# Optimization experiments

Hardware: AMD Instinct MI355X
Metric: run time of the kernel (lower is better)

The kernel has to match this reference:

```python
import jax, jax.numpy as jnp
import numpy as np

N_WIRES = 8
DIM = 2 ** N_WIRES  # 256
NUM_HEADS = 4

def _cnot_ring_perm():
    # Compose CNOT(w, w+1) for w=0..6 then CNOT(7, 0) into one basis permutation.
    # Wire 0 is the most-significant bit of the basis index.
    perm = np.arange(DIM)
    pairs = [(w, w + 1) for w in range(N_WIRES - 1)] + [(N_WIRES - 1, 0)]
    j = np.arange(DIM)
    for c, t in pairs:
        ctrl = (j >> (N_WIRES - 1 - c)) & 1
        M = j ^ (ctrl << (N_WIRES - 1 - t))  # flip target bit where control=1 (involution)
        perm = perm[M]
    return perm

PERM = _cnot_ring_perm()
# SIGNS[i, w] = <i|Z_w|i> = 1 - 2*bit_w(i)
SIGNS = np.array([[1.0 - 2.0 * ((i >> (N_WIRES - 1 - w)) & 1) for w in range(N_WIRES)]
                  for i in range(DIM)], dtype=np.float32)

def setup_inputs() -> dict:
    key = jax.random.key(0)
    k1, k2, k3 = jax.random.split(key, 3)
    x = jax.random.normal(k1, (16, 4096, N_WIRES), jnp.float32)  # rotation angles per token
    theta = jax.random.normal(k2, (N_WIRES,), jnp.float32)       # trainable RX params
    w_combine = jax.random.normal(k3, (N_WIRES, N_WIRES), jnp.float32) / np.float32(np.sqrt(N_WIRES))
    b_combine = jnp.zeros((N_WIRES,), jnp.float32)
    return {"x": x, "theta": theta, "w_combine": w_combine, "b_combine": b_combine}

def _quantum_features(x, theta):
    # RX(x_i) then RX(theta_i) on wire i compose to RX(x_i + theta_i) acting on |0>.
    B, S, E = x.shape
    N = B * S
    phi = (x + theta).reshape(N, E)
    c = jnp.cos(0.5 * phi).astype(jnp.complex64)
    s = (-1j) * jnp.sin(0.5 * phi)          # RX|0> = cos(phi/2)|0> - i sin(phi/2)|1>
    wv = jnp.stack([c, s.astype(jnp.complex64)], axis=-1)  # (N, 8, 2)
    # Build product state via successive Kronecker products (wire 0 = MSB).
    state = jnp.ones((N, 1), jnp.complex64)
    for w in range(E):
        state = (state[:, :, None] * wv[:, w, None, :]).reshape(N, -1)  # (N, 2^(w+1))
    state = state[:, jnp.asarray(PERM)]      # apply the CNOT ring as one permutation
    probs = state.real ** 2 + state.imag ** 2  # (N, 256)
    return (probs @ jnp.asarray(SIGNS)).reshape(B, S, E)  # <Z_w> per token

def reference(x, theta, w_combine, b_combine):
    B, S, E = x.shape
    d_k = E // NUM_HEADS
    q = _quantum_features(x, theta)           # (B, S, 8); k = v = q in the source
    scores = jnp.einsum('bse,bte->bst', q, q) / np.float32(np.sqrt(d_k))
    attn = jax.nn.softmax(scores, axis=-1)    # dropout is identity in eval mode
    out = jnp.einsum('bst,bte->bse', attn, q)
    # Faithful to source: transpose(1,2).contiguous().view(B, S, E)
    out = jnp.swapaxes(out, 1, 2).reshape(B, S, E)
    return out @ w_combine.T + b_combine
```

## Files before the change

### kernel.cpp

```cpp
#include <hip/hip_runtime.h>
#include <math.h>


#define SEQ   4096
#define NB    16
#define SROWS 128
#define TPB   1024
#define NTG   4
#define TC    1024
#define NCH   (SEQ / TC)
#define TILES_PER_TG 8
#define KSTR  12
#define VSTR  1032

typedef _Float16 f16x4  __attribute__((ext_vector_type(4)));
typedef _Float16 f16x8  __attribute__((ext_vector_type(8)));
typedef float    f32x16 __attribute__((ext_vector_type(16)));
typedef __fp16   hf2    __attribute__((ext_vector_type(2)));

#if __has_builtin(__builtin_amdgcn_exp2f)
#define EXP2F(x) __builtin_amdgcn_exp2f(x)
#else
#define EXP2F(x) exp2f(x)
#endif

__global__ __launch_bounds__(TPB, 8)
void qattn_kernel(const float* __restrict__ x, const float* __restrict__ theta,
                  const float* __restrict__ wc, const float* __restrict__ bc,
                  float* __restrict__ out)
{
    __shared__ __align__(16) _Float16 kf[TC * KSTR];
    __shared__ __align__(16) _Float16 vt[9 * VSTR];
    float* part = (float*)kf;
    float* attn = (float*)vt;

    const int tid  = threadIdx.x;
    const int lane = tid & 63;
    const int wv   = tid >> 6;
    const int sub  = wv & 3;
    const int tg   = wv >> 2;
    const int l31  = lane & 31;
    const int hp   = lane >> 5;

    const int b  = blockIdx.x >> 5;
    const int S0 = (blockIdx.x & 31) * SROWS;
    const float* xb = x + (size_t)b * SEQ * 8;

    const int pos = (tid & ~12) | ((tid & 4) << 1) | ((tid & 8) >> 1);

    float th[8];
#pragma unroll
    for (int w = 0; w < 8; ++w) th[w] = theta[w];

    vt[8 * VSTR + tid] = (_Float16)1.0f;

    f16x4 qfrag;
    {
        const int s = S0 + sub * 32 + l31;
        const float4 xa  = *(const float4*)(xb + s * 8);
        const float4 xb4 = *(const float4*)(xb + s * 8 + 4);
        float c0 = __cosf(xa.x  + th[0]);
        float c1 = __cosf(xa.y  + th[1]);
        float c2 = __cosf(xa.z  + th[2]);
        float c3 = __cosf(xa.w  + th[3]);
        float c4 = __cosf(xb4.x + th[4]);
        float c5 = __cosf(xb4.y + th[5]);
        float c6 = __cosf(xb4.z + th[6]);
        float c7 = __cosf(xb4.w + th[7]);
        float p1 = c0 * c1, p2 = p1 * c2, p3 = p2 * c3, p4 = p3 * c4;
        float p5 = p4 * c5, p6 = p5 * c6, p7 = p6 * c7;
        float p0 = c1 * c2 * c3 * c4 * c5 * c6 * c7;
        const float sc = 0.70710678118654752f * 1.44269504088896341f;
        if (hp == 0)
            qfrag = (f16x4){(_Float16)(p0*sc), (_Float16)(p1*sc),
                            (_Float16)(p2*sc), (_Float16)(p3*sc)};
        else
            qfrag = (f16x4){(_Float16)(p4*sc), (_Float16)(p5*sc),
                            (_Float16)(p6*sc), (_Float16)(p7*sc)};
    }

    f32x16 o = {0.f,0.f,0.f,0.f,0.f,0.f,0.f,0.f,0.f,0.f,0.f,0.f,0.f,0.f,0.f,0.f};

    const int wr = (l31 < 8) ? l31 : 8;
    const _Float16* kfb = kf + l31 * KSTR + 4 * hp + (tg * TILES_PER_TG) * 32 * KSTR;
    const _Float16* vbb = vt + wr * VSTR + 8 * hp + tg * (TILES_PER_TG * 32);

    float4 pxa = *(const float4*)(xb + tid * 8);
    float4 pxb = *(const float4*)(xb + tid * 8 + 4);

    for (int ch = 0; ch < NCH; ++ch) {
        float c0 = __cosf(pxa.x + th[0]);
        float c1 = __cosf(pxa.y + th[1]);
        float c2 = __cosf(pxa.z + th[2]);
        float c3 = __cosf(pxa.w + th[3]);
        float c4 = __cosf(pxb.x + th[4]);
        float c5 = __cosf(pxb.y + th[5]);
        float c6 = __cosf(pxb.z + th[6]);
        float c7 = __cosf(pxb.w + th[7]);
        float p1 = c0 * c1, p2 = p1 * c2, p3 = p2 * c3, p4 = p3 * c4;
        float p5 = p4 * c5, p6 = p5 * c6, p7 = p6 * c7;
        float p0 = c1 * c2 * c3 * c4 * c5 * c6 * c7;
        _Float16 h0 = (_Float16)p0, h1 = (_Float16)p1, h2 = (_Float16)p2,
                 h3 = (_Float16)p3, h4 = (_Float16)p4, h5 = (_Float16)p5,
                 h6 = (_Float16)p6, h7 = (_Float16)p7;
        __syncthreads();
        {
            _Float16* krow = kf + tid * KSTR;
            *(f16x4*)(krow)     = (f16x4){h0, h1, h2, h3};
            *(f16x4*)(krow + 4) = (f16x4){h4, h5, h6, h7};
            vt[0 * VSTR + pos] = h0;
            vt[1 * VSTR + pos] = h1;
            vt[2 * VSTR + pos] = h2;
            vt[3 * VSTR + pos] = h3;
            vt[4 * VSTR + pos] = h4;
            vt[5 * VSTR + pos] = h5;
            vt[6 * VSTR + pos] = h6;
            vt[7 * VSTR + pos] = h7;
        }
        __syncthreads();
        {
            const int nt = ((ch + 1 < NCH) ? (ch + 1) * TC : ch * TC) + tid;
            pxa = *(const float4*)(xb + nt * 8);
            pxb = *(const float4*)(xb + nt * 8 + 4);
        }
#pragma unroll 4
        for (int i = 0; i < TILES_PER_TG; ++i) {
            f16x4 kfrag = *(const f16x4*)(kfb + i * 32 * KSTR);
            f32x16 cc = __builtin_amdgcn_mfma_f32_32x32x8f16(
                kfrag, qfrag, (f32x16){0.f,0.f,0.f,0.f,0.f,0.f,0.f,0.f,
                                       0.f,0.f,0.f,0.f,0.f,0.f,0.f,0.f}, 0, 0, 0);
#pragma unroll
            for (int h = 0; h < 2; ++h) {
                union { hf2 q[4]; f16x8 v; } pa;
                pa.q[0] = __builtin_amdgcn_cvt_pkrtz(EXP2F(cc[8*h+0]), EXP2F(cc[8*h+1]));
                pa.q[1] = __builtin_amdgcn_cvt_pkrtz(EXP2F(cc[8*h+2]), EXP2F(cc[8*h+3]));
                pa.q[2] = __builtin_amdgcn_cvt_pkrtz(EXP2F(cc[8*h+4]), EXP2F(cc[8*h+5]));
                pa.q[3] = __builtin_amdgcn_cvt_pkrtz(EXP2F(cc[8*h+6]), EXP2F(cc[8*h+7]));
                f16x8 vfrag = *(const f16x8*)(vbb + i * 32 + h * 16);
                o = __builtin_amdgcn_mfma_f32_32x32x16_f16(pa.v, vfrag, o, 0, 0, 0);
            }
        }
    }

    __syncthreads();
    if (l31 < 9) {
#pragma unroll
        for (int r = 0; r < 16; ++r) {
            const int sloc = sub * 32 + (r & 3) + 8 * (r >> 2) + 4 * hp;
            part[((tg * SROWS) + sloc) * 9 + l31] = o[r];
        }
    }
    __syncthreads();
    for (int idx = tid; idx < SROWS * 9; idx += TPB) {
        const int rr = idx / 9;
        const int w  = idx - rr * 9;
        float sm = 0.f;
#pragma unroll
        for (int g = 0; g < NTG; ++g) sm += part[((g * SROWS) + rr) * 9 + w];
        attn[rr * 9 + w] = sm;
    }
    __syncthreads();
    if (tid < SROWS * 8) {
        const int rr = tid >> 3;
        const int w  = tid & 7;
        attn[rr * 9 + w] = attn[rr * 9 + w] / attn[rr * 9 + 8];
    }
    __syncthreads();

    if (tid < SROWS) {
        const int e    = tid >> 4;
        const int nloc = tid & 15;
        const int r    = e * 512 + (S0 >> 3) + nloc;
        float y[8];
#pragma unroll
        for (int c = 0; c < 8; ++c) y[c] = attn[(nloc * 8 + c) * 9 + e];
        float oo[8];
#pragma unroll
        for (int k = 0; k < 8; ++k) {
            float a = bc[k];
#pragma unroll
            for (int c = 0; c < 8; ++c) a += y[c] * wc[k * 8 + c];
            oo[k] = a;
        }
        float4* op = (float4*)(out + ((size_t)b * SEQ + r) * 8);
        op[0] = make_float4(oo[0], oo[1], oo[2], oo[3]);
        op[1] = make_float4(oo[4], oo[5], oo[6], oo[7]);
    }
}

extern "C" void kernel_launch(void* const* d_in, const int* in_sizes, int n_in,
                              void* d_out, int out_size, void* d_ws, size_t ws_size,
                              hipStream_t stream)
{
    const float* x  = (const float*)d_in[0];
    const float* th = (const float*)d_in[1];
    const float* wc = (const float*)d_in[2];
    const float* bc = (const float*)d_in[3];
    float* out = (float*)d_out;

    qattn_kernel<<<dim3(NB * (SEQ / SROWS)), dim3(TPB), 0, stream>>>(x, th, wc, bc, out);
}
```

Before: 92.37 us.

## Double-buffer K/V tiles in shared memory with halved chunk size

Splits the key/value chunk from 1024 to 512 tokens and double-buffers the shared-memory K and V tiles. Each iteration stages the next chunk while computing MFMAs on the current one, leaving one barrier per chunk instead of two. Only half the threads do the staging, and the loop runs twice as many chunks. Shared-memory footprint stays about the same, so occupancy should be unchanged.

After: 88.19 us. -4.5%, faster.

```diff
diff --git a/kernel.cpp b/kernel.cpp
--- a/kernel.cpp
+++ b/kernel.cpp
@@ -7,11 +7,13 @@
 #define SROWS 128
 #define TPB   1024
 #define NTG   4
-#define TC    1024
+#define TC    512
 #define NCH   (SEQ / TC)
-#define TILES_PER_TG 8
+#define TPT   4
 #define KSTR  12
-#define VSTR  1032
+#define VSTR  520
+#define KFSZ  (TC * KSTR)
+#define VTSZ  (9 * VSTR)
 
 typedef _Float16 f16x4  __attribute__((ext_vector_type(4)));
 typedef _Float16 f16x8  __attribute__((ext_vector_type(8)));
@@ -29,8 +31,8 @@
                   const float* __restrict__ wc, const float* __restrict__ bc,
                   float* __restrict__ out)
 {
-    __shared__ __align__(16) _Float16 kf[TC * KSTR];
-    __shared__ __align__(16) _Float16 vt[9 * VSTR];
+    __shared__ __align__(16) _Float16 kf[2 * KFSZ];
+    __shared__ __align__(16) _Float16 vt[2 * VTSZ];
     float* part = (float*)kf;
     float* attn = (float*)vt;
 
@@ -51,8 +53,6 @@
     float th[8];
 #pragma unroll
     for (int w = 0; w < 8; ++w) th[w] = theta[w];
-
-    vt[8 * VSTR + tid] = (_Float16)1.0f;
 
     f16x4 qfrag;
     {
@@ -79,52 +79,64 @@
                             (_Float16)(p6*sc), (_Float16)(p7*sc)};
     }
 
-    f32x16 o = {0.f,0.f,0.f,0.f,0.f,0.f,0.f,0.f,0.f,0.f,0.f,0.f,0.f,0.f,0.f,0.f};
-
-    const int wr = (l31 < 8) ? l31 : 8;
-    const _Float16* kfb = kf + l31 * KSTR + 4 * hp + (tg * TILES_PER_TG) * 32 * KSTR;
-    const _Float16* vbb = vt + wr * VSTR + 8 * hp + tg * (TILES_PER_TG * 32);
-
-    float4 pxa = *(const float4*)(xb + tid * 8);
-    float4 pxb = *(const float4*)(xb + tid * 8 + 4);
-
-    for (int ch = 0; ch < NCH; ++ch) {
-        float c0 = __cosf(pxa.x + th[0]);
-        float c1 = __cosf(pxa.y + th[1]);
-        float c2 = __cosf(pxa.z + th[2]);
-        float c3 = __cosf(pxa.w + th[3]);
-        float c4 = __cosf(pxb.x + th[4]);
-        float c5 = __cosf(pxb.y + th[5]);
-        float c6 = __cosf(pxb.z + th[6]);
-        float c7 = __cosf(pxb.w + th[7]);
+    auto stage = [&](int buf, float4 xa, float4 xb4) {
+        float c0 = __cosf(xa.x  + th[0]);
+        float c1 = __cosf(xa.y  + th[1]);
+        float c2 = __cosf(xa.z  + th[2]);
+        float c3 = __cosf(xa.w  + th[3]);
+        float c4 = __cosf(xb4.x + th[4]);
+        float c5 = __cosf(xb4.y + th[5]);
+        float c6 = __cosf(xb4.z + th[6]);
+        float c7 = __cosf(xb4.w + th[7]);
         float p1 = c0 * c1, p2 = p1 * c2, p3 = p2 * c3, p4 = p3 * c4;
         float p5 = p4 * c5, p6 = p5 * c6, p7 = p6 * c7;
         float p0 = c1 * c2 * c3 * c4 * c5 * c6 * c7;
         _Float16 h0 = (_Float16)p0, h1 = (_Float16)p1, h2 = (_Float16)p2,
                  h3 = (_Float16)p3, h4 = (_Float16)p4, h5 = (_Float16)p5,
                  h6 = (_Float16)p6, h7 = (_Float16)p7;
-        __syncthreads();
-        {
-            _Float16* krow = kf + tid * KSTR;
-            *(f16x4*)(krow)     = (f16x4){h0, h1, h2, h3};
-            *(f16x4*)(krow + 4) = (f16x4){h4, h5, h6, h7};
-            vt[0 * VSTR + pos] = h0;
-            vt[1 * VSTR + pos] = h1;
-            vt[2 * VSTR + pos] = h2;
-            vt[3 * VSTR + pos] = h3;
-            vt[4 * VSTR + pos] = h4;
-            vt[5 * VSTR + pos] = h5;
-            vt[6 * VSTR + pos] = h6;
-            vt[7 * VSTR + pos] = h7;
-        }
-        __syncthreads();
-        {
-            const int nt = ((ch + 1 < NCH) ? (ch + 1) * TC : ch * TC) + tid;
-            pxa = *(const float4*)(xb + nt * 8);
-            pxb = *(const float4*)(xb + nt * 8 + 4);
-        }
-#pragma unroll 4
-        for (int i = 0; i < TILES_PER_TG; ++i) {
+        _Float16* krow = kf + buf * KFSZ + tid * KSTR;
+        *(f16x4*)(krow)     = (f16x4){h0, h1, h2, h3};
+        *(f16x4*)(krow + 4) = (f16x4){h4, h5, h6, h7};
+        _Float16* vb = vt + buf * VTSZ + pos;
+        vb[0 * VSTR] = h0;
+        vb[1 * VSTR] = h1;
+        vb[2 * VSTR] = h2;
+        vb[3 * VSTR] = h3;
+        vb[4 * VSTR] = h4;
+        vb[5 * VSTR] = h5;
+        vb[6 * VSTR] = h6;
+        vb[7 * VSTR] = h7;
+    };
+
+    float4 pxa, pxb;
+    if (tid < TC) {
+        vt[0 * VTSZ + 8 * VSTR + tid] = (_Float16)1.0f;
+        vt[1 * VTSZ + 8 * VSTR + tid] = (_Float16)1.0f;
+        const float4 xa  = *(const float4*)(xb + tid * 8);
+        const float4 xb4 = *(const float4*)(xb + tid * 8 + 4);
+        stage(0, xa, xb4);
+        pxa = *(const float4*)(xb + (TC + tid) * 8);
+        pxb = *(const float4*)(xb + (TC + tid) * 8 + 4);
+    }
+
+    f32x16 o = {0.f,0.f,0.f,0.f,0.f,0.f,0.f,0.f,0.f,0.f,0.f,0.f,0.f,0.f,0.f,0.f};
+
+    const int wr = (l31 < 8) ? l31 : 8;
+    __syncthreads();
+
+    for (int ch = 0; ch < NCH; ++ch) {
+        const int c = ch & 1;
+        if (ch + 1 < NCH && tid < TC) {
+            stage(c ^ 1, pxa, pxb);
+        }
+        if (ch + 2 < NCH && tid < TC) {
+            pxa = *(const float4*)(xb + ((ch + 2) * TC + tid) * 8);
+            pxb = *(const float4*)(xb + ((ch + 2) * TC + tid) * 8 + 4);
+        }
+        const _Float16* kfb = kf + c * KFSZ + l31 * KSTR + 4 * hp + tg * (TPT * 32) * KSTR;
+        const _Float16* vbb = vt + c * VTSZ + wr * VSTR + 8 * hp + tg * (TPT * 32);
+#pragma unroll
+        for (int i = 0; i < TPT; ++i) {
             f16x4 kfrag = *(const f16x4*)(kfb + i * 32 * KSTR);
             f32x16 cc = __builtin_amdgcn_mfma_f32_32x32x8f16(
                 kfrag, qfrag, (f32x16){0.f,0.f,0.f,0.f,0.f,0.f,0.f,0.f,
@@ -140,9 +152,9 @@
                 o = __builtin_amdgcn_mfma_f32_32x32x16_f16(pa.v, vfrag, o, 0, 0, 0);
             }
         }
-    }
-
-    __syncthreads();
+        __syncthreads();
+    }
+
     if (l31 < 9) {
 #pragma unroll
         for (int r = 0; r < 16; ++r) {
```
